# Optimization experiments

Hardware: AMD Instinct MI355X
Metric: run time of the kernel (lower is better)

## Reference

```python
import jax, jax.numpy as jnp
import numpy as np

D = 1024
H = 16
HD = D // H
MLP = 4 * D
EPS = 1e-5


def layernorm(x, g, b):
    mu = jnp.mean(x, axis=-1, keepdims=True)
    var = jnp.mean(jnp.square(x - mu), axis=-1, keepdims=True)
    return (x - mu) * jax.lax.rsqrt(var + EPS) * g + b


def setup_inputs() -> dict:
    key = jax.random.key(0)
    ks = jax.random.split(key, 12)
    s = 0.02
    return {
        "x": jax.random.normal(ks[0], (2, 2048, D), jnp.float32),
        "ln1_g": jnp.ones((D,), jnp.float32),
        "ln1_b": jnp.zeros((D,), jnp.float32),
        "lnm_g": jnp.ones((D,), jnp.float32),
        "lnm_b": jnp.zeros((D,), jnp.float32),
        "qkv_w": jax.random.normal(ks[1], (D, 3 * D), jnp.float32) * s,
        "qkv_b": jnp.zeros((3 * D,), jnp.float32),
        "proj_w": jax.random.normal(ks[2], (D, D), jnp.float32) * s,
        "proj_b": jnp.zeros((D,), jnp.float32),
        "fc1_w": jax.random.normal(ks[3], (D, MLP), jnp.float32) * s,
        "fc1_b": jnp.zeros((MLP,), jnp.float32),
        "fc2_w": jax.random.normal(ks[4], (MLP, D), jnp.float32) * s,
        "fc2_b": jnp.zeros((D,), jnp.float32),
    }


def reference(x, ln1_g, ln1_b, lnm_g, lnm_b, qkv_w, qkv_b, proj_w, proj_b,
              fc1_w, fc1_b, fc2_w, fc2_b):
    B, N, _ = x.shape
    scale = HD ** -0.5
    # --- self-attention on norm1(x) ---
    h = layernorm(x, ln1_g, ln1_b)
    qkv = h @ qkv_w + qkv_b                       # [B, N, 3D]
    qkv = qkv.reshape(B, N, 3, H, HD)
    q, k, v = qkv[:, :, 0], qkv[:, :, 1], qkv[:, :, 2]  # [B, N, H, HD]
    attn = jnp.einsum("bqhd,bkhd->bhqk", q, k) * scale
    attn = jax.nn.softmax(attn, axis=-1)
    o = jnp.einsum("bhqk,bkhd->bqhd", attn, v).reshape(B, N, D)
    x = x + (o @ proj_w + proj_b)
    # --- MLP ---
    m = layernorm(x, lnm_g, lnm_b)
    m = jax.nn.gelu(m @ fc1_w + fc1_b, approximate=False)
    x = x + (m @ fc2_w + fc2_b)
    return x
```

## Files before the change

kernel.cpp:

```cpp
#include <hip/hip_runtime.h>

typedef __bf16 bf16_t;
typedef bf16_t bf16x4 __attribute__((ext_vector_type(4)));
typedef bf16_t bf16x8 __attribute__((ext_vector_type(8)));
typedef float f32x4 __attribute__((ext_vector_type(4)));
typedef unsigned short u16x8 __attribute__((ext_vector_type(8)));

#define MFMA(a, b, c) __builtin_amdgcn_mfma_f32_16x16x32_bf16(a, b, c, 0, 0, 0)

__device__ inline float exp2_fast(float x) {
  float r;
  asm volatile("v_exp_f32 %0, %1" : "=v"(r) : "v"(x));
  return r;
}

__device__ inline void gll16(const bf16_t* g, bf16_t* l) {
  __builtin_amdgcn_global_load_lds(
      (const __attribute__((address_space(1))) unsigned int*)(g),
      (__attribute__((address_space(3))) unsigned int*)(l), 16, 0, 0);
}

__device__ inline float gelu_f(float v) {
  float ax = fabsf(v) * 0.70710678118f;
  float t = __builtin_amdgcn_rcpf(1.0f + 0.3275911f * ax);
  float p = ((((1.061405429f * t - 1.453152027f) * t + 1.421413741f) * t -
              0.284496736f) * t + 0.254829592f) * t;
  float e = exp2_fast(-ax * ax * 1.4426950408889634f);
  float erf = 1.0f - p * e;
  erf = v < 0.f ? -erf : erf;
  return 0.5f * v * (1.0f + erf);
}

__global__ __launch_bounds__(256) void wconv_all(
    const float* __restrict__ qkv_w, bf16_t* __restrict__ qkv_wt,
    const float* __restrict__ proj_w, bf16_t* __restrict__ proj_wt,
    const float* __restrict__ fc1_w, bf16_t* __restrict__ fc1_wt,
    const float* __restrict__ fc2_w, bf16_t* __restrict__ fc2_wt,
    const float* __restrict__ x, const float* __restrict__ g1,
    const float* __restrict__ b1, bf16_t* __restrict__ h) {
  int id = blockIdx.x;
  if (id >= 3072) {
    long row = id - 3072;
    const float4* xr = (const float4*)(x + row * 1024);
    float4 v = xr[threadIdx.x];
    float s = v.x + v.y + v.z + v.w;
    float s2 = v.x * v.x + v.y * v.y + v.z * v.z + v.w * v.w;
#pragma unroll
    for (int m = 32; m >= 1; m >>= 1) {
      s += __shfl_xor(s, m);
      s2 += __shfl_xor(s2, m);
    }
    __shared__ float red[8];
    int wid = threadIdx.x >> 6;
    if ((threadIdx.x & 63) == 0) {
      red[wid] = s;
      red[4 + wid] = s2;
    }
    __syncthreads();
    s = red[0] + red[1] + red[2] + red[3];
    s2 = red[4] + red[5] + red[6] + red[7];
    float mu = s * (1.f / 1024.f);
    float rs = rsqrtf(s2 * (1.f / 1024.f) - mu * mu + 1e-5f);
    float4 gv = ((const float4*)g1)[threadIdx.x];
    float4 bv = ((const float4*)b1)[threadIdx.x];
    bf16_t o0 = (bf16_t)((v.x - mu) * rs * gv.x + bv.x);
    bf16_t o1 = (bf16_t)((v.y - mu) * rs * gv.y + bv.y);
    bf16_t o2 = (bf16_t)((v.z - mu) * rs * gv.z + bv.z);
    bf16_t o3 = (bf16_t)((v.w - mu) * rs * gv.w + bv.w);
    ushort4 pk;
    pk.x = *(unsigned short*)&o0;
    pk.y = *(unsigned short*)&o1;
    pk.z = *(unsigned short*)&o2;
    pk.w = *(unsigned short*)&o3;
    *(ushort4*)(h + row * 1024 + threadIdx.x * 4) = pk;
    return;
  }
  const float* W;
  bf16_t* Wt;
  int K, N, bx, by;
  if (id < 768) {
    W = qkv_w; Wt = qkv_wt; K = 1024; N = 3072; bx = id % 48; by = id / 48;
  } else if (id < 1024) {
    int l = id - 768;
    W = proj_w; Wt = proj_wt; K = 1024; N = 1024; bx = l % 16; by = l / 16;
  } else if (id < 2048) {
    int l = id - 1024;
    W = fc1_w; Wt = fc1_wt; K = 1024; N = 4096; bx = l % 64; by = l / 64;
  } else {
    int l = id - 2048;
    W = fc2_w; Wt = fc2_wt; K = 4096; N = 1024; bx = l % 16; by = l / 16;
  }
  __shared__ float t[64][65];
  int n0 = bx * 64, k0 = by * 64;
  int tid = threadIdx.x;
  int c4 = tid & 15;
  int r = tid >> 4;
#pragma unroll
  for (int s = 0; s < 4; s++) {
    int k = r + s * 16;
    float4 v = *(const float4*)(W + (long)(k0 + k) * N + n0 + c4 * 4);
    t[k][c4 * 4] = v.x;
    t[k][c4 * 4 + 1] = v.y;
    t[k][c4 * 4 + 2] = v.z;
    t[k][c4 * 4 + 3] = v.w;
  }
  __syncthreads();
  int n = tid >> 2;
  int kc = (tid & 3) * 16;
  ushort4 pk[4];
#pragma unroll
  for (int c = 0; c < 4; c++) {
#pragma unroll
    for (int j = 0; j < 4; j++) {
      bf16_t xq = (bf16_t)t[kc + c * 4 + j][n];
      ((unsigned short*)&pk[c])[j] = *(unsigned short*)&xq;
    }
  }
  bf16_t* dst = Wt + (long)(n0 + n) * K + k0 + kc;
#pragma unroll
  for (int c = 0; c < 4; c++) *(ushort4*)(dst + c * 4) = pk[c];
}

#define STAGE_PTR(DA, DB, k0)                 \
  gll16(ga + (k0), DA + w * 512);             \
  gll16(ga + (k0) + astep, DA + 4096 + w * 512); \
  gll16(gb + (k0), DB + w * 512);

#define COMPUTE(LA, LB)                                                \
  {                                                                    \
    bf16x8 af[4], bfr[4];                                              \
    _Pragma("unroll") for (int mt = 0; mt < 4; mt++) af[mt] =          \
        *(const bf16x8*)(LA + (wm + mt * 16 + l15) * 32 + quad * 8);   \
    _Pragma("unroll") for (int nt = 0; nt < 4; nt++) bfr[nt] =         \
        *(const bf16x8*)(LB + (wn + nt * 16 + l15) * 32 + quad * 8);   \
    _Pragma("unroll") for (int mt = 0; mt < 4; mt++)                   \
        _Pragma("unroll") for (int nt = 0; nt < 4; nt++) acc[mt][nt] = \
            MFMA(af[mt], bfr[nt], acc[mt][nt]);                        \
  }

#define WB3 asm volatile("s_waitcnt vmcnt(3)\ns_barrier" ::: "memory")
#define WB0 asm volatile("s_waitcnt vmcnt(0)\ns_barrier" ::: "memory")

__global__ __launch_bounds__(512, 4) void gemm_kernel(
    const bf16_t* __restrict__ A, const bf16_t* __restrict__ Bt,
    const float* __restrict__ bias, const float* __restrict__ resid,
    void* __restrict__ Cout, int M, int N, int K, int epi, int nbn, int nz) {
  __shared__ bf16_t lA0[256 * 32], lB0[128 * 32];
  __shared__ bf16_t lA1[256 * 32], lB1[128 * 32];
  __shared__ bf16_t lA2[256 * 32], lB2[128 * 32];
  int tid = threadIdx.x;
  int id = blockIdx.x;
  int xcd = id & 7;
  int slot = id >> 3;
  int gpx = (nbn * nz) >> 3;
  int g = xcd * gpx + (slot >> 4);
  int bm = slot & 15;
  int bn = g / nz;
  int kz = g % nz;
  int kchunk = K / nz;
  int kbeg = kz * kchunk, kend = kbeg + kchunk;

  int lane = tid & 63, w = tid >> 6;
  int quad = lane >> 4, l15 = lane & 15;
  int wm = (w & 3) * 64, wn = (w >> 2) * 64;

  f32x4 acc[4][4];
#pragma unroll
  for (int i = 0; i < 4; i++)
#pragma unroll
    for (int j = 0; j < 4; j++) acc[i][j] = (f32x4){0.f, 0.f, 0.f, 0.f};

  const bf16_t* ga = A + (long)(bm * 256 + w * 16 + (lane >> 2)) * K + (lane & 3) * 8;
  const bf16_t* gb = Bt + (long)(bn * 128 + w * 16 + (lane >> 2)) * K + (lane & 3) * 8;
  long astep = (long)128 * K;

  int nit = (kend - kbeg) >> 5;
  bf16_t *A0 = lA0, *A1 = lA1, *A2 = lA2;
  bf16_t *B0 = lB0, *B1 = lB1, *B2 = lB2;
  STAGE_PTR(A0, B0, kbeg);
  STAGE_PTR(A1, B1, kbeg + 32);
  for (int i = 0; i < nit; i++) {
    if (i + 1 < nit) { WB3; } else { WB0; }
    if (i + 2 < nit) {
      int ks = kbeg + (i + 2) * 32;
      STAGE_PTR(A2, B2, ks);
    }
    COMPUTE(A0, B0);
    bf16_t* t;
    t = A0; A0 = A1; A1 = A2; A2 = t;
    t = B0; B0 = B1; B1 = B2; B2 = t;
  }

#pragma unroll
  for (int mt = 0; mt < 4; mt++) {
#pragma unroll
    for (int r = 0; r < 4; r++) {
      long row = bm * 256 + wm + mt * 16 + quad * 4 + r;
#pragma unroll
      for (int nt = 0; nt < 4; nt++) {
        int col = bn * 128 + wn + nt * 16 + l15;
        long idx = row * N + col;
        if (epi == 3) {
          ((bf16_t*)Cout)[(long)kz * M * N + idx] = (bf16_t)acc[mt][nt][r];
        } else {
          float v = acc[mt][nt][r] + bias[col];
          if (epi == 1) {
            ((float*)Cout)[idx] = v + resid[idx];
          } else if (epi == 2) {
            ((bf16_t*)Cout)[idx] = (bf16_t)gelu_f(v);
          } else {
            ((bf16_t*)Cout)[idx] = (bf16_t)v;
          }
        }
      }
    }
  }
}

__global__ __launch_bounds__(256) void reduce_ln_kernel(
    const bf16_t* __restrict__ p, const float* __restrict__ bias,
    const float* __restrict__ resid, float* __restrict__ x1,
    const float* __restrict__ g, const float* __restrict__ bb,
    bf16_t* __restrict__ mb) {
  const long MN = (long)4096 * 1024;
  long row = blockIdx.x;
  int t = threadIdx.x;
  bf16x4 a0 = *(const bf16x4*)(p + row * 1024 + t * 4);
  bf16x4 a1 = *(const bf16x4*)(p + MN + row * 1024 + t * 4);
  bf16x4 a2 = *(const bf16x4*)(p + 2 * MN + row * 1024 + t * 4);
  bf16x4 a3 = *(const bf16x4*)(p + 3 * MN + row * 1024 + t * 4);
  float4 r = ((const float4*)(resid + row * 1024))[t];
  float4 bv = ((const float4*)bias)[t];
  float4 v;
  v.x = (float)a0[0] + (float)a1[0] + (float)a2[0] + (float)a3[0] + r.x + bv.x;
  v.y = (float)a0[1] + (float)a1[1] + (float)a2[1] + (float)a3[1] + r.y + bv.y;
  v.z = (float)a0[2] + (float)a1[2] + (float)a2[2] + (float)a3[2] + r.z + bv.z;
  v.w = (float)a0[3] + (float)a1[3] + (float)a2[3] + (float)a3[3] + r.w + bv.w;
  ((float4*)(x1 + row * 1024))[t] = v;
  float s = v.x + v.y + v.z + v.w;
  float s2 = v.x * v.x + v.y * v.y + v.z * v.z + v.w * v.w;
#pragma unroll
  for (int m = 32; m >= 1; m >>= 1) {
    s += __shfl_xor(s, m);
    s2 += __shfl_xor(s2, m);
  }
  __shared__ float red[8];
  int wid = t >> 6;
  if ((t & 63) == 0) {
    red[wid] = s;
    red[4 + wid] = s2;
  }
  __syncthreads();
  s = red[0] + red[1] + red[2] + red[3];
  s2 = red[4] + red[5] + red[6] + red[7];
  float mu = s * (1.f / 1024.f);
  float rs = rsqrtf(s2 * (1.f / 1024.f) - mu * mu + 1e-5f);
  float4 gv = ((const float4*)g)[t];
  float4 b2 = ((const float4*)bb)[t];
  bf16_t o0 = (bf16_t)((v.x - mu) * rs * gv.x + b2.x);
  bf16_t o1 = (bf16_t)((v.y - mu) * rs * gv.y + b2.y);
  bf16_t o2 = (bf16_t)((v.z - mu) * rs * gv.z + b2.z);
  bf16_t o3 = (bf16_t)((v.w - mu) * rs * gv.w + b2.w);
  ushort4 pk;
  pk.x = *(unsigned short*)&o0;
  pk.y = *(unsigned short*)&o1;
  pk.z = *(unsigned short*)&o2;
  pk.w = *(unsigned short*)&o3;
  *(ushort4*)(mb + row * 1024 + t * 4) = pk;
}

__global__ __launch_bounds__(256) void reduce4_kernel(const bf16_t* __restrict__ p,
                                                      const float* __restrict__ bias,
                                                      const float* __restrict__ resid,
                                                      float* __restrict__ out) {
  long i = (long)blockIdx.x * 256 + threadIdx.x;
  const long MN = (long)4096 * 1024;
  bf16x4 a0 = *(const bf16x4*)(p + i * 4);
  bf16x4 a1 = *(const bf16x4*)(p + MN + i * 4);
  bf16x4 a2 = *(const bf16x4*)(p + 2 * MN + i * 4);
  bf16x4 a3 = *(const bf16x4*)(p + 3 * MN + i * 4);
  float4 r = ((const float4*)resid)[i];
  float4 bv = ((const float4*)bias)[i & 255];
  float4 o;
  o.x = (float)a0[0] + (float)a1[0] + (float)a2[0] + (float)a3[0] + r.x + bv.x;
  o.y = (float)a0[1] + (float)a1[1] + (float)a2[1] + (float)a3[1] + r.y + bv.y;
  o.z = (float)a0[2] + (float)a1[2] + (float)a2[2] + (float)a3[2] + r.z + bv.z;
  o.w = (float)a0[3] + (float)a1[3] + (float)a2[3] + (float)a3[3] + r.w + bv.w;
  ((float4*)out)[i] = o;
}

#define LDV 72

__global__ __launch_bounds__(256) void attn_kernel(const bf16_t* __restrict__ qkv,
                                                   bf16_t* __restrict__ o) {
  const int LD = 3072;
  int id = blockIdx.x;
  int within = id >> 3;
  int bh = (id & 7) * 4 + (within >> 4);
  int qt = within & 15;
  int h = bh & 15, b = bh >> 4;

  int tid = threadIdx.x, w = tid >> 6, lane = tid & 63;
  int quad = lane >> 4, l15 = lane & 15;
  int qrow = qt * 128 + w * 32;
  const bf16_t* base = qkv + (long)b * 2048 * LD + h * 64;
  const bf16_t* Qp = base;
  const bf16_t* Kp = base + 1024;
  const bf16_t* Vp = base + 2048;

  __shared__ bf16_t lK[2][64 * 64];
  __shared__ bf16_t lV[2][64 * LDV];
  __shared__ bf16_t lP[4][32 * LDV];
  bf16_t* myp = lP[w];

  const bf16_t* kg =
      Kp + (long)(w * 16 + (lane >> 3)) * LD + (((lane & 7) ^ (lane >> 3)) & 7) * 8;
  int kk = tid & 31;
  int d0 = (tid >> 5) * 8;
  const bf16_t* vg = Vp + (long)(2 * kk) * LD + d0;

  gll16(kg, lK[0] + w * 1024);
  gll16(kg + 8 * (long)LD, lK[0] + w * 1024 + 512);
  u16x8 va = *(const u16x8*)(vg);
  u16x8 vb = *(const u16x8*)(vg + LD);

  const float c2 = 0.18033688011112042f;
  bf16x8 qf[2][2];
#pragma unroll
  for (int qi = 0; qi < 2; qi++)
#pragma unroll
    for (int d = 0; d < 2; d++) {
      bf16x8 q0 =
          *(const bf16x8*)(Qp + (long)(qrow + qi * 16 + l15) * LD + d * 32 + quad * 8);
#pragma unroll
      for (int j = 0; j < 8; j++) qf[qi][d][j] = (bf16_t)((float)q0[j] * c2);
    }

  f32x4 oacc[2][4];
#pragma unroll
  for (int qi = 0; qi < 2; qi++)
#pragma unroll
    for (int t = 0; t < 4; t++) oacc[qi][t] = (f32x4){0.f, 0.f, 0.f, 0.f};
  float li_p[2][4] = {{0.f, 0.f, 0.f, 0.f}, {0.f, 0.f, 0.f, 0.f}};

  int sw0 = (quad ^ l15) & 7;
  int sw1 = ((quad + 4) ^ l15) & 7;

  for (int it = 0; it < 32; it++) {
    int cur = it & 1, nxt = cur ^ 1;
    asm volatile("s_waitcnt vmcnt(0)\ns_barrier" ::: "memory");
    unsigned int* lvw = (unsigned int*)lV[cur];
#pragma unroll
    for (int j = 0; j < 8; j++)
      lvw[(d0 + j) * (LDV / 2) + kk] = (unsigned int)va[j] | ((unsigned int)vb[j] << 16);
    u16x8 va_n = va, vb_n = vb;
    if (it + 1 < 32) {
      long koff2 = (long)(it + 1) * 64 * LD;
      gll16(kg + koff2, lK[nxt] + w * 1024);
      gll16(kg + koff2 + 8 * (long)LD, lK[nxt] + w * 1024 + 512);
      va_n = *(const u16x8*)(vg + koff2);
      vb_n = *(const u16x8*)(vg + koff2 + LD);
    }
    asm volatile("s_waitcnt lgkmcnt(0)\ns_barrier" ::: "memory");

    bf16x8 kf[4][2];
#pragma unroll
    for (int st = 0; st < 4; st++) {
      const bf16_t* krow = lK[cur] + (st * 16 + l15) * 64;
      kf[st][0] = *(const bf16x8*)(krow + sw0 * 8);
      kf[st][1] = *(const bf16x8*)(krow + sw1 * 8);
    }
    f32x4 s[2][4];
#pragma unroll
    for (int qi = 0; qi < 2; qi++)
#pragma unroll
      for (int st = 0; st < 4; st++) {
        f32x4 z = (f32x4){0.f, 0.f, 0.f, 0.f};
        z = MFMA(qf[qi][0], kf[st][0], z);
        s[qi][st] = MFMA(qf[qi][1], kf[st][1], z);
      }

#pragma unroll
    for (int qi = 0; qi < 2; qi++)
#pragma unroll
      for (int st = 0; st < 4; st++)
#pragma unroll
        for (int r = 0; r < 4; r++) {
          float p = exp2_fast(s[qi][st][r]);
          s[qi][st][r] = p;
          li_p[qi][r] += p;
        }

#pragma unroll
    for (int qi = 0; qi < 2; qi++)
#pragma unroll
      for (int r = 0; r < 4; r++)
#pragma unroll
        for (int st = 0; st < 4; st++)
          myp[(qi * 16 + quad * 4 + r) * LDV + st * 16 + l15] = (bf16_t)s[qi][st][r];
    asm volatile("s_waitcnt lgkmcnt(0)" ::: "memory");

    bf16x8 pa[2][2];
#pragma unroll
    for (int qi = 0; qi < 2; qi++) {
      pa[qi][0] = *(const bf16x8*)(myp + (qi * 16 + l15) * LDV + quad * 8);
      pa[qi][1] = *(const bf16x8*)(myp + (qi * 16 + l15) * LDV + 32 + quad * 8);
    }
#pragma unroll
    for (int t = 0; t < 4; t++) {
      const bf16_t* vr = lV[cur] + (t * 16 + l15) * LDV + quad * 8;
      bf16x8 v0 = *(const bf16x8*)(vr);
      bf16x8 v1 = *(const bf16x8*)(vr + 32);
#pragma unroll
      for (int qi = 0; qi < 2; qi++) {
        oacc[qi][t] = MFMA(pa[qi][0], v0, oacc[qi][t]);
        oacc[qi][t] = MFMA(pa[qi][1], v1, oacc[qi][t]);
      }
    }
    va = va_n;
    vb = vb_n;
  }

#pragma unroll
  for (int qi = 0; qi < 2; qi++) {
    float li[4];
#pragma unroll
    for (int r = 0; r < 4; r++) {
      float s = li_p[qi][r];
#pragma unroll
      for (int x = 8; x >= 1; x >>= 1) s += __shfl_xor(s, x);
      li[r] = s;
    }
#pragma unroll
    for (int t = 0; t < 4; t++)
#pragma unroll
      for (int r = 0; r < 4; r++) {
        long q = qrow + qi * 16 + quad * 4 + r;
        o[((long)b * 2048 + q) * 1024 + h * 64 + t * 16 + l15] =
            (bf16_t)(oacc[qi][t][r] / li[r]);
      }
  }
}

extern "C" void kernel_launch(void* const* d_in, const int* in_sizes, int n_in,
                              void* d_out, int out_size, void* d_ws, size_t ws_size,
                              hipStream_t stream) {
  (void)in_sizes; (void)n_in; (void)out_size; (void)ws_size;
  const float* x = (const float*)d_in[0];
  const float* ln1_g = (const float*)d_in[1];
  const float* ln1_b = (const float*)d_in[2];
  const float* lnm_g = (const float*)d_in[3];
  const float* lnm_b = (const float*)d_in[4];
  const float* qkv_w = (const float*)d_in[5];
  const float* qkv_b = (const float*)d_in[6];
  const float* proj_w = (const float*)d_in[7];
  const float* proj_b = (const float*)d_in[8];
  const float* fc1_w = (const float*)d_in[9];
  const float* fc1_b = (const float*)d_in[10];
  const float* fc2_w = (const float*)d_in[11];
  const float* fc2_b = (const float*)d_in[12];
  float* out = (float*)d_out;

  const int M = 4096;
  const int D_ = 1024, MLP_ = 4096, QKV = 3072;

  char* ws = (char*)d_ws;
  bf16_t* h = (bf16_t*)(ws);
  bf16_t* qkvb = (bf16_t*)(ws + (8u << 20));
  bf16_t* ob = (bf16_t*)(ws + (32u << 20));
  float* x1 = (float*)(ws + (40u << 20));
  bf16_t* mb = (bf16_t*)(ws + (56u << 20));
  bf16_t* gb = (bf16_t*)(ws + (64u << 20));
  bf16_t* qkv_wt = (bf16_t*)(ws + (96u << 20));
  bf16_t* proj_wt = (bf16_t*)(ws + (102u << 20));
  bf16_t* fc1_wt = (bf16_t*)(ws + (104u << 20));
  bf16_t* fc2_wt = (bf16_t*)(ws + (112u << 20));
  bf16_t* p_proj = (bf16_t*)(ws);
  bf16_t* p_fc2 = (bf16_t*)(ws);

  wconv_all<<<7168, 256, 0, stream>>>(qkv_w, qkv_wt, proj_w, proj_wt, fc1_w, fc1_wt,
                                      fc2_w, fc2_wt, x, ln1_g, ln1_b, h);
  gemm_kernel<<<384, 512, 0, stream>>>(h, qkv_wt, qkv_b, nullptr, qkvb, M, QKV, D_, 0,
                                       24, 1);
  attn_kernel<<<512, 256, 0, stream>>>(qkvb, ob);
  gemm_kernel<<<512, 512, 0, stream>>>(ob, proj_wt, nullptr, nullptr, p_proj, M, D_,
                                       D_, 3, 8, 4);
  reduce_ln_kernel<<<M, 256, 0, stream>>>(p_proj, proj_b, x, x1, lnm_g, lnm_b, mb);
  gemm_kernel<<<512, 512, 0, stream>>>(mb, fc1_wt, fc1_b, nullptr, gb, M, MLP_, D_, 2,
                                       32, 1);
  gemm_kernel<<<512, 512, 0, stream>>>(gb, fc2_wt, nullptr, nullptr, p_fc2, M, D_,
                                       MLP_, 3, 8, 4);
  reduce4_kernel<<<4096, 256, 0, stream>>>(p_fc2, fc2_b, x1, out);
}
```

Before: 384.6 us.

## Pre-transpose V into per-head layout and stream it into LDS asynchronously

Adds a small kernel that transposes V from the packed QKV buffer into a [batch, head, dim, key] layout in workspace. The attention kernel then loads V tiles with direct global-to-LDS loads and the same swizzle as K, replacing register staging and per-thread LDS transposed writes. This also drops one barrier per iteration. The trade-off is an extra kernel launch plus an extra round trip of V through global memory.

```diff
diff --git a/kernel.cpp b/kernel.cpp
--- a/kernel.cpp
+++ b/kernel.cpp
@@ -4,7 +4,6 @@
 typedef bf16_t bf16x4 __attribute__((ext_vector_type(4)));
 typedef bf16_t bf16x8 __attribute__((ext_vector_type(8)));
 typedef float f32x4 __attribute__((ext_vector_type(4)));
-typedef unsigned short u16x8 __attribute__((ext_vector_type(8)));
 
 #define MFMA(a, b, c) __builtin_amdgcn_mfma_f32_16x16x32_bf16(a, b, c, 0, 0, 0)
 
@@ -119,6 +118,43 @@
   bf16_t* dst = Wt + (long)(n0 + n) * K + k0 + kc;
 #pragma unroll
   for (int c = 0; c < 4; c++) *(ushort4*)(dst + c * 4) = pk[c];
+}
+
+__global__ __launch_bounds__(256) void vt_kernel(const bf16_t* __restrict__ qkvb,
+                                                 bf16_t* __restrict__ vt) {
+  int id = blockIdx.x;
+  int kt = id & 31;
+  int h = (id >> 5) & 15;
+  int b = id >> 9;
+  const bf16_t* src = qkvb + ((long)b * 2048 + kt * 64) * 3072 + 2048 + h * 64;
+  bf16_t* dst = vt + ((long)(b * 16 + h) * 64) * 2048 + kt * 64;
+  __shared__ bf16_t lt[64][65];
+  int tid = threadIdx.x;
+  int c4 = tid & 15;
+  int r = tid >> 4;
+#pragma unroll
+  for (int s = 0; s < 4; s++) {
+    int k = r + s * 16;
+    ushort4 v = *(const ushort4*)(src + (long)k * 3072 + c4 * 4);
+    lt[k][c4 * 4] = *(bf16_t*)&v.x;
+    lt[k][c4 * 4 + 1] = *(bf16_t*)&v.y;
+    lt[k][c4 * 4 + 2] = *(bf16_t*)&v.z;
+    lt[k][c4 * 4 + 3] = *(bf16_t*)&v.w;
+  }
+  __syncthreads();
+  int n = tid >> 2;
+  int kc = (tid & 3) * 16;
+  ushort4 pk[4];
+#pragma unroll
+  for (int c = 0; c < 4; c++) {
+#pragma unroll
+    for (int j = 0; j < 4; j++) {
+      bf16_t xq = lt[kc + c * 4 + j][n];
+      ((unsigned short*)&pk[c])[j] = *(unsigned short*)&xq;
+    }
+  }
+#pragma unroll
+  for (int c = 0; c < 4; c++) *(ushort4*)(dst + (long)n * 2048 + kc + c * 4) = pk[c];
 }
 
 #define STAGE_PTR(DA, DB, k0)                 \
@@ -292,6 +328,7 @@
 #define LDV 72
 
 __global__ __launch_bounds__(256) void attn_kernel(const bf16_t* __restrict__ qkv,
+                                                   const bf16_t* __restrict__ vt,
                                                    bf16_t* __restrict__ o) {
   const int LD = 3072;
   int id = blockIdx.x;
@@ -306,23 +343,22 @@
   const bf16_t* base = qkv + (long)b * 2048 * LD + h * 64;
   const bf16_t* Qp = base;
   const bf16_t* Kp = base + 1024;
-  const bf16_t* Vp = base + 2048;
+  const bf16_t* Vtp = vt + (long)(b * 16 + h) * 64 * 2048;
 
   __shared__ bf16_t lK[2][64 * 64];
-  __shared__ bf16_t lV[2][64 * LDV];
+  __shared__ bf16_t lVt[2][64 * 64];
   __shared__ bf16_t lP[4][32 * LDV];
   bf16_t* myp = lP[w];
 
   const bf16_t* kg =
       Kp + (long)(w * 16 + (lane >> 3)) * LD + (((lane & 7) ^ (lane >> 3)) & 7) * 8;
-  int kk = tid & 31;
-  int d0 = (tid >> 5) * 8;
-  const bf16_t* vg = Vp + (long)(2 * kk) * LD + d0;
+  const bf16_t* vg =
+      Vtp + (long)(w * 16 + (lane >> 3)) * 2048 + (((lane & 7) ^ (lane >> 3)) & 7) * 8;
 
   gll16(kg, lK[0] + w * 1024);
   gll16(kg + 8 * (long)LD, lK[0] + w * 1024 + 512);
-  u16x8 va = *(const u16x8*)(vg);
-  u16x8 vb = *(const u16x8*)(vg + LD);
+  gll16(vg, lVt[0] + w * 1024);
+  gll16(vg + 8 * 2048, lVt[0] + w * 1024 + 512);
 
   const float c2 = 0.18033688011112042f;
   bf16x8 qf[2][2];
@@ -349,19 +385,13 @@
   for (int it = 0; it < 32; it++) {
     int cur = it & 1, nxt = cur ^ 1;
     asm volatile("s_waitcnt vmcnt(0)\ns_barrier" ::: "memory");
-    unsigned int* lvw = (unsigned int*)lV[cur];
-#pragma unroll
-    for (int j = 0; j < 8; j++)
-      lvw[(d0 + j) * (LDV / 2) + kk] = (unsigned int)va[j] | ((unsigned int)vb[j] << 16);
-    u16x8 va_n = va, vb_n = vb;
     if (it + 1 < 32) {
-      long koff2 = (long)(it + 1) * 64 * LD;
-      gll16(kg + koff2, lK[nxt] + w * 1024);
-      gll16(kg + koff2 + 8 * (long)LD, lK[nxt] + w * 1024 + 512);
-      va_n = *(const u16x8*)(vg + koff2);
-      vb_n = *(const u16x8*)(vg + koff2 + LD);
-    }
-    asm volatile("s_waitcnt lgkmcnt(0)\ns_barrier" ::: "memory");
+      long ko = (long)(it + 1) * 64;
+      gll16(kg + ko * LD, lK[nxt] + w * 1024);
+      gll16(kg + ko * LD + 8 * (long)LD, lK[nxt] + w * 1024 + 512);
+      gll16(vg + ko, lVt[nxt] + w * 1024);
+      gll16(vg + ko + 8 * 2048, lVt[nxt] + w * 1024 + 512);
+    }
 
     bf16x8 kf[4][2];
 #pragma unroll
@@ -408,17 +438,15 @@
     }
 #pragma unroll
     for (int t = 0; t < 4; t++) {
-      const bf16_t* vr = lV[cur] + (t * 16 + l15) * LDV + quad * 8;
-      bf16x8 v0 = *(const bf16x8*)(vr);
-      bf16x8 v1 = *(const bf16x8*)(vr + 32);
+      const bf16_t* vr = lVt[cur] + (t * 16 + l15) * 64;
+      bf16x8 v0 = *(const bf16x8*)(vr + sw0 * 8);
+      bf16x8 v1 = *(const bf16x8*)(vr + sw1 * 8);
 #pragma unroll
       for (int qi = 0; qi < 2; qi++) {
         oacc[qi][t] = MFMA(pa[qi][0], v0, oacc[qi][t]);
         oacc[qi][t] = MFMA(pa[qi][1], v1, oacc[qi][t]);
       }
     }
-    va = va_n;
-    vb = vb_n;
   }
 
 #pragma unroll
@@ -475,6 +503,7 @@
   bf16_t* proj_wt = (bf16_t*)(ws + (102u << 20));
   bf16_t* fc1_wt = (bf16_t*)(ws + (104u << 20));
   bf16_t* fc2_wt = (bf16_t*)(ws + (112u << 20));
+  bf16_t* vt = (bf16_t*)(ws + (120u << 20));
   bf16_t* p_proj = (bf16_t*)(ws);
   bf16_t* p_fc2 = (bf16_t*)(ws);
 
@@ -482,7 +511,8 @@
                                       fc2_w, fc2_wt, x, ln1_g, ln1_b, h);
   gemm_kernel<<<384, 512, 0, stream>>>(h, qkv_wt, qkv_b, nullptr, qkvb, M, QKV, D_, 0,
                                        24, 1);
-  attn_kernel<<<512, 256, 0, stream>>>(qkvb, ob);
+  vt_kernel<<<1024, 256, 0, stream>>>(qkvb, vt);
+  attn_kernel<<<512, 256, 0, stream>>>(qkvb, vt, ob);
   gemm_kernel<<<512, 512, 0, stream>>>(ob, proj_wt, nullptr, nullptr, p_proj, M, D_,
                                        D_, 3, 8, 4);
   reduce_ln_kernel<<<M, 256, 0, stream>>>(p_proj, proj_b, x, x1, lnm_g, lnm_b, mb);
```

New measurement: 387.8 us. About the same (+0.8%).
